# Kernel optimization log

Measured on AMD Instinct MI355X. Metric: run time of the kernel, lower is better.

The kernel has to match this reference:

```python
import jax, jax.numpy as jnp
import numpy as np


def setup_inputs() -> dict:
    key = jax.random.key(0)
    k1, k2, k3 = jax.random.split(key, 3)
    S, B, H, D = 1024, 32, 512, 1024  # max_len, batch, bin_rnn_size, bin_rep_size
    hidden = jax.random.normal(k1, (2, B, H), dtype=jnp.float32)
    encoder_outputs = jax.random.normal(k2, (S, B, D), dtype=jnp.float32)
    # nn.Linear(D, D) params; scale W for numerically sane softmax logits
    W = jax.random.normal(k3, (D, D), dtype=jnp.float32) / np.float32(np.sqrt(D))
    b = jnp.zeros((D,), dtype=jnp.float32)
    return {"hidden": hidden, "encoder_outputs": encoder_outputs, "W": W, "b": b}


def reference(hidden, encoder_outputs, W, b):
    # method == 'general'
    B = hidden.shape[1]
    # torch.reshape((-1, B, 2H)).squeeze() == C-order flatten -> [B, 2H]
    h = hidden.reshape(B, -1)                                   # [B, D]
    energy = jnp.einsum('sbd,ed->sbe', encoder_outputs, W) + b  # Linear: x @ W.T + b
    # batch_product_luong + sum over features == contraction
    attn_energies = jnp.einsum('bd,sbd->bs', h, energy)         # [B, S]
    alpha = jax.nn.softmax(attn_energies, axis=1)[:, None, :]   # [B, 1, S]
    # alpha.bmm(encoder_outputs.transpose(0,1)) -> [B, 1, D]
    reps = jnp.einsum('bos,sbd->bod', alpha, encoder_outputs)
    return (reps, alpha)
```

## Files before the change

### kernel.cpp

```cpp
#include <hip/hip_runtime.h>

#define S 1024
#define B 32
#define D 1024
#define NCH 32
#define CH (S / NCH)
#define ECH 16
#define EC (D / ECH)

__global__ __launch_bounds__(256) void k1_gW(const float* __restrict__ hid,
                                             const float* __restrict__ W,
                                             float* __restrict__ g) {
    const int tid = threadIdx.x;
    const int d   = blockIdx.x * 256 + tid;
    const int e0  = blockIdx.y * EC;
    __shared__ float4 sh[EC * 8];
    for (int k = 0; k < (EC * 32) / 256; ++k) {
        int lin = tid + k * 256;
        int b = lin >> 6;
        int e = lin & (EC - 1);
        ((float*)sh)[e * 32 + b] = hid[b * D + e0 + e];
    }
    __syncthreads();
    float acc[32];
    #pragma unroll
    for (int b = 0; b < 32; ++b) acc[b] = 0.f;
    for (int e = 0; e < EC; ++e) {
        float w = W[(size_t)(e0 + e) * D + d];
        #pragma unroll
        for (int j = 0; j < 8; ++j) {
            float4 hv = sh[e * 8 + j];
            acc[4 * j + 0] += hv.x * w;
            acc[4 * j + 1] += hv.y * w;
            acc[4 * j + 2] += hv.z * w;
            acc[4 * j + 3] += hv.w * w;
        }
    }
    #pragma unroll
    for (int b = 0; b < 32; ++b) atomicAdd(&g[b * D + d], acc[b]);
}

__global__ __launch_bounds__(256) void k2_fused(const float* __restrict__ enc,
                                                const float* __restrict__ g,
                                                float* __restrict__ logits,
                                                float* __restrict__ marr,
                                                float* __restrict__ larr,
                                                float* __restrict__ pacc) {
    const int tid  = threadIdx.x;
    const int c    = blockIdx.x;
    const int b    = blockIdx.y;
    const int lane = tid & 63;
    const int wid  = tid >> 6;
    __shared__ float red[2][4];
    const float4 gv = ((const float4*)(g + b * D))[tid];
    const float4* encb = (const float4*)enc;
    size_t base = ((size_t)(c * CH) * B + b) * (D / 4) + tid;
    float4 ecur = encb[base];
    float m = -3.0e38f, l = 0.f;
    float4 acc = {0.f, 0.f, 0.f, 0.f};
    for (int i = 0; i < CH; ++i) {
        float4 enx = ecur;
        if (i + 1 < CH) enx = encb[base + (size_t)(i + 1) * B * (D / 4)];
        float pd = ecur.x * gv.x + ecur.y * gv.y + ecur.z * gv.z + ecur.w * gv.w;
        #pragma unroll
        for (int off = 32; off > 0; off >>= 1)
            pd += __shfl_down(pd, off, 64);
        if (lane == 0) red[i & 1][wid] = pd;
        __syncthreads();
        float logit = red[i & 1][0] + red[i & 1][1] + red[i & 1][2] + red[i & 1][3];
        if (tid == 0) logits[b * S + c * CH + i] = logit;
        float mn = fmaxf(m, logit);
        float sc = __expf(m - mn);
        float p  = __expf(logit - mn);
        l = l * sc + p;
        acc.x = acc.x * sc + p * ecur.x;
        acc.y = acc.y * sc + p * ecur.y;
        acc.z = acc.z * sc + p * ecur.z;
        acc.w = acc.w * sc + p * ecur.w;
        m = mn;
        ecur = enx;
    }
    ((float4*)pacc)[(size_t)(c * B + b) * (D / 4) + tid] = acc;
    if (tid == 0) { marr[c * B + b] = m; larr[c * B + b] = l; }
}

__global__ __launch_bounds__(256) void k3_combine(const float* __restrict__ logits,
                                                  const float* __restrict__ marr,
                                                  const float* __restrict__ larr,
                                                  const float* __restrict__ pacc,
                                                  float* __restrict__ out) {
    const int tid = threadIdx.x;
    const int q   = blockIdx.x;
    const int b   = blockIdx.y;
    __shared__ float shm[NCH], shl[NCH];
    if (tid < NCH) { shm[tid] = marr[tid * B + b]; shl[tid] = larr[tid * B + b]; }
    __syncthreads();
    float mg = -3.0e38f;
    #pragma unroll
    for (int c = 0; c < NCH; ++c) mg = fmaxf(mg, shm[c]);
    const int d = q * 256 + tid;
    float lg = 0.f, racc = 0.f;
    #pragma unroll 4
    for (int c = 0; c < NCH; ++c) {
        float fc = __expf(shm[c] - mg);
        lg   += shl[c] * fc;
        racc += pacc[(size_t)(c * B + b) * D + d] * fc;
    }
    float inv = 1.f / lg;
    out[b * D + d] = racc * inv;
    int s = q * 256 + tid;
    out[B * D + b * S + s] = __expf(logits[b * S + s] - mg) * inv;
}

extern "C" void kernel_launch(void* const* d_in, const int* in_sizes, int n_in,
                              void* d_out, int out_size, void* d_ws, size_t ws_size,
                              hipStream_t stream) {
    const float* hid = (const float*)d_in[0];
    const float* enc = (const float*)d_in[1];
    const float* W   = (const float*)d_in[2];

    float* out = (float*)d_out;

    float* g      = (float*)d_ws;
    float* logits = g + B * D;
    float* marr   = logits + B * S;
    float* larr   = marr + NCH * B;
    float* pacc   = larr + NCH * B;

    hipMemsetAsync(g, 0, B * D * sizeof(float), stream);
    k1_gW<<<dim3(D / 256, ECH), 256, 0, stream>>>(hid, W, g);
    k2_fused<<<dim3(NCH, B), 256, 0, stream>>>(enc, g, logits, marr, larr, pacc);
    k3_combine<<<dim3(4, B), 256, 0, stream>>>(logits, marr, larr, pacc, out);
}
```

Measured before the change: 51.07 us.

## Give each wavefront its own rows in fused attention kernel, removing per-row block sync

In the fused kernel, each of the four wavefronts now handles its own subset of rows, and each lane holds four float4 slices of the 1024-wide row. The row dot product is reduced entirely inside the wavefront with xor shuffles, which removes the per-row __syncthreads and shared-memory reduction. The per-wave online-softmax partials are merged through shared memory once at the end. This costs more registers per thread and a final 16KB shared merge, and each wave now runs a serial loop of only 8 rows.

```diff
diff --git a/kernel.cpp b/kernel.cpp
--- a/kernel.cpp
+++ b/kernel.cpp
@@ -5,6 +5,7 @@
 #define D 1024
 #define NCH 32
 #define CH (S / NCH)
+#define RPW (CH / 4)
 #define ECH 16
 #define EC (D / ECH)
 
@@ -47,41 +48,77 @@
                                                 float* __restrict__ larr,
                                                 float* __restrict__ pacc) {
     const int tid  = threadIdx.x;
+    const int lane = tid & 63;
+    const int wid  = tid >> 6;
     const int c    = blockIdx.x;
     const int b    = blockIdx.y;
-    const int lane = tid & 63;
-    const int wid  = tid >> 6;
-    __shared__ float red[2][4];
-    const float4 gv = ((const float4*)(g + b * D))[tid];
+
+    const float4* gp = (const float4*)(g + b * D);
+    float4 gv[4];
+    #pragma unroll
+    for (int j = 0; j < 4; ++j) gv[j] = gp[j * 64 + lane];
+
     const float4* encb = (const float4*)enc;
-    size_t base = ((size_t)(c * CH) * B + b) * (D / 4) + tid;
-    float4 ecur = encb[base];
+    const int row0 = c * CH + wid * RPW;
+    const size_t rstride = (size_t)B * (D / 4);
+    size_t base = ((size_t)row0 * B + b) * (D / 4) + lane;
+
+    float4 cur[4], nxt[4];
+    #pragma unroll
+    for (int j = 0; j < 4; ++j) cur[j] = encb[base + j * 64];
+
     float m = -3.0e38f, l = 0.f;
-    float4 acc = {0.f, 0.f, 0.f, 0.f};
-    for (int i = 0; i < CH; ++i) {
-        float4 enx = ecur;
-        if (i + 1 < CH) enx = encb[base + (size_t)(i + 1) * B * (D / 4)];
-        float pd = ecur.x * gv.x + ecur.y * gv.y + ecur.z * gv.z + ecur.w * gv.w;
+    float4 acc[4] = {{0,0,0,0},{0,0,0,0},{0,0,0,0},{0,0,0,0}};
+
+    for (int i = 0; i < RPW; ++i) {
+        if (i + 1 < RPW) {
+            size_t nb = base + (size_t)(i + 1) * rstride;
+            #pragma unroll
+            for (int j = 0; j < 4; ++j) nxt[j] = encb[nb + j * 64];
+        }
+        float pd = 0.f;
         #pragma unroll
-        for (int off = 32; off > 0; off >>= 1)
-            pd += __shfl_down(pd, off, 64);
-        if (lane == 0) red[i & 1][wid] = pd;
-        __syncthreads();
-        float logit = red[i & 1][0] + red[i & 1][1] + red[i & 1][2] + red[i & 1][3];
-        if (tid == 0) logits[b * S + c * CH + i] = logit;
-        float mn = fmaxf(m, logit);
+        for (int j = 0; j < 4; ++j)
+            pd += cur[j].x * gv[j].x + cur[j].y * gv[j].y +
+                  cur[j].z * gv[j].z + cur[j].w * gv[j].w;
+        #pragma unroll
+        for (int off = 1; off < 64; off <<= 1)
+            pd += __shfl_xor(pd, off, 64);
+        if (lane == 0) logits[b * S + row0 + i] = pd;
+        float mn = fmaxf(m, pd);
         float sc = __expf(m - mn);
-        float p  = __expf(logit - mn);
+        float p  = __expf(pd - mn);
         l = l * sc + p;
-        acc.x = acc.x * sc + p * ecur.x;
-        acc.y = acc.y * sc + p * ecur.y;
-        acc.z = acc.z * sc + p * ecur.z;
-        acc.w = acc.w * sc + p * ecur.w;
+        #pragma unroll
+        for (int j = 0; j < 4; ++j) {
+            acc[j].x = acc[j].x * sc + p * cur[j].x;
+            acc[j].y = acc[j].y * sc + p * cur[j].y;
+            acc[j].z = acc[j].z * sc + p * cur[j].z;
+            acc[j].w = acc[j].w * sc + p * cur[j].w;
+        }
         m = mn;
-        ecur = enx;
+        #pragma unroll
+        for (int j = 0; j < 4; ++j) cur[j] = nxt[j];
     }
-    ((float4*)pacc)[(size_t)(c * B + b) * (D / 4) + tid] = acc;
-    if (tid == 0) { marr[c * B + b] = m; larr[c * B + b] = l; }
+
+    __shared__ float4 sacc[4][256];
+    __shared__ float  sm[4], sl[4];
+    #pragma unroll
+    for (int j = 0; j < 4; ++j) sacc[wid][j * 64 + lane] = acc[j];
+    if (lane == 0) { sm[wid] = m; sl[wid] = l; }
+    __syncthreads();
+    float mg = fmaxf(fmaxf(sm[0], sm[1]), fmaxf(sm[2], sm[3]));
+    float4 r = {0, 0, 0, 0};
+    float lsum = 0.f;
+    #pragma unroll
+    for (int w = 0; w < 4; ++w) {
+        float fw = __expf(sm[w] - mg);
+        float4 a = sacc[w][wid * 64 + lane];
+        r.x += a.x * fw; r.y += a.y * fw; r.z += a.z * fw; r.w += a.w * fw;
+        lsum += sl[w] * fw;
+    }
+    ((float4*)pacc)[(size_t)(c * B + b) * (D / 4) + wid * 64 + lane] = r;
+    if (tid == 0) { marr[c * B + b] = mg; larr[c * B + b] = lsum; }
 }
 
 __global__ __launch_bounds__(256) void k3_combine(const float* __restrict__ logits,
```

After: 51.53 us. Within noise of the previous version (+0.9%).
